# Optimization experiments

Hardware: AMD Instinct MI355X
Metric: run time of the kernel (lower is better)

## Reference

```python
import jax, jax.numpy as jnp
import numpy as np

EPS = 1e-12

def _l2norm(v, axis=-1):
    n = jnp.sqrt(jnp.sum(v * v, axis=axis, keepdims=True))
    return v / jnp.maximum(n, EPS)

def setup_inputs() -> dict:
    key = jax.random.key(0)
    ks = jax.random.split(key, 6)
    B, S, E, A = 256, 128, 768, 30
    x = jax.random.normal(ks[0], (B, S, E), dtype=jnp.float32)
    W_att = jax.random.normal(ks[1], (E, E), dtype=jnp.float32) * (1.0 / np.sqrt(E))
    b_att = jnp.zeros((E,), dtype=jnp.float32)
    W_red = jax.random.normal(ks[2], (E, A), dtype=jnp.float32) * (1.0 / np.sqrt(E))
    b_red = jnp.zeros((A,), dtype=jnp.float32)
    aspect_W = jax.random.normal(ks[3], (A, E), dtype=jnp.float32) * (1.0 / np.sqrt(E))
    # negatives: uniform over other batch elements (multinomial on ones - eye)
    idx = jax.random.randint(ks[4], (B, 10), 0, B - 1)
    neg_idx = (idx + (idx >= jnp.arange(B)[:, None])).astype(jnp.int32)  # skip self
    return {"x": x, "W_att": W_att, "b_att": b_att, "W_red": W_red,
            "b_red": b_red, "aspect_W": aspect_W, "neg_idx": neg_idx}

def reference(x, W_att, b_att, W_red, b_red, aspect_W, neg_idx):
    # --- LuongAttention(general): query = mean over seq ---
    q = x.mean(axis=1)                                   # [B,E]
    qW = q @ W_att + b_att                               # [B,E]
    scores = jnp.einsum('bse,be->bs', x, qW)             # [B,S]
    attn = jax.nn.softmax(scores, axis=-1)
    z_s = jnp.einsum('bs,bse->be', attn, x)              # attended sentence vec [B,E]
    # --- reduction + reconstruction ---
    composition = jax.nn.softmax(z_s @ W_red + b_red, axis=-1)  # [B,A]
    reconstructed = composition @ aspect_W                      # [B,E]
    # --- max-margin loss with gathered negatives ---
    r_s = _l2norm(reconstructed)                         # F.normalize
    z_n = z_s[neg_idx]                                   # [B,10,E] gather
    pos = jnp.einsum('be,be->b', z_s, r_s)[:, None]      # [B,1]
    negs = jnp.einsum('bne,be->bn', z_n, r_s)            # [B,10]
    J = 1.0 - pos + negs
    margin_loss = jnp.mean(jnp.maximum(J, 0.0))
    # --- orthogonal regularization on aspect embeddings ---
    T_n = _l2norm(aspect_W, axis=1)                      # [A,E]
    G = T_n @ T_n.T - jnp.eye(aspect_W.shape[0], dtype=aspect_W.dtype)
    reg = jnp.sqrt(jnp.sum(G * G))                       # Frobenius norm
    loss = reg + margin_loss
    return (z_s, reconstructed, loss)
```

## Files before the change

### kernel.cpp

```cpp
#include <hip/hip_runtime.h>
#include <hip/hip_bf16.h>
#include <hip/hip_fp16.h>
#include <math.h>

#define B 256
#define S 128
#define E 768
#define E4 192
#define NA 30
#define NNEG 10

#define K2_KC 96
#define K2_KR 192

__device__ __forceinline__ float dot4(float4 a, float4 b) {
    return a.x * b.x + a.y * b.y + a.z * b.z + a.w * b.w;
}
__device__ __forceinline__ float wave_reduce_sum(float v) {
#pragma unroll
    for (int off = 32; off; off >>= 1) v += __shfl_down(v, off);
    return v;
}
__device__ __forceinline__ float wave_reduce_max(float v) {
#pragma unroll
    for (int off = 32; off; off >>= 1) v = fmaxf(v, __shfl_down(v, off));
    return v;
}
__device__ __forceinline__ float4 h4_to_f4(uint2 p) {
    __half2* ph = (__half2*)&p;
    float2 f0 = __half22float2(ph[0]);
    float2 f1 = __half22float2(ph[1]);
    return make_float4(f0.x, f0.y, f1.x, f1.y);
}

template <int USE16>
__global__ __launch_bounds__(768) void mean_prep_kernel(const float* __restrict__ x,
                                                        const float* __restrict__ W_red,
                                                        const float* __restrict__ aspect_W,
                                                        float* __restrict__ q,
                                                        float* __restrict__ WredT,
                                                        float* __restrict__ invn,
                                                        __half* __restrict__ xh) {
    int bid = blockIdx.x;
    int tid = threadIdx.x;
    __shared__ __align__(16) float4 part[4][E4];
    __shared__ float red[12];

    if (bid < 2 * B) {
        int b = bid >> 1, half = bid & 1;
        int c = tid % E4;
        int g = tid / E4;
        const float4* xb = (const float4*)(x + (size_t)b * S * E);
        uint2* xhb = (uint2*)(xh + (size_t)b * S * E);
        int s0 = half * 64 + g * 16;
        float4 acc = make_float4(0.f, 0.f, 0.f, 0.f);
#pragma unroll 4
        for (int s = s0; s < s0 + 16; ++s) {
            float4 v = xb[(size_t)s * E4 + c];
            acc.x += v.x; acc.y += v.y; acc.z += v.z; acc.w += v.w;
            if (USE16) {
                __half2 h01 = __floats2half2_rn(v.x, v.y);
                __half2 h23 = __floats2half2_rn(v.z, v.w);
                uint2 pk;
                pk.x = *(unsigned int*)&h01;
                pk.y = *(unsigned int*)&h23;
                xhb[(size_t)s * E4 + c] = pk;
            }
        }
        part[g][c] = acc;
        __syncthreads();
        if (tid < E4) {
            float4 a0 = part[0][c], a1 = part[1][c], a2 = part[2][c], a3 = part[3][c];
            const float inv = 1.0f / (float)S;
            float4 r;
            r.x = (a0.x + a1.x + a2.x + a3.x) * inv;
            r.y = (a0.y + a1.y + a2.y + a3.y) * inv;
            r.z = (a0.z + a1.z + a2.z + a3.z) * inv;
            r.w = (a0.w + a1.w + a2.w + a3.w) * inv;
            ((float4*)q)[((size_t)half * B + b) * E4 + c] = r;
        }
    } else {
        int a = bid - 2 * B;
        WredT[(size_t)a * E + tid] = W_red[(size_t)tid * NA + a];
        int wave = tid >> 6, lane = tid & 63;
        float v = aspect_W[(size_t)a * E + tid];
        float ss = wave_reduce_sum(v * v);
        if (lane == 0) red[wave] = ss;
        __syncthreads();
        if (tid == 0) {
            float n = 0.f;
#pragma unroll
            for (int w = 0; w < 12; ++w) n += red[w];
            invn[a] = 1.0f / fmaxf(sqrtf(n), 1e-12f);
        }
    }
}

__global__ __launch_bounds__(256) void qw_partial_kernel(const float* __restrict__ q,
                                                         const float* __restrict__ W_att,
                                                         float* __restrict__ part) {
    int b0 = blockIdx.x * 64;
    int e0 = blockIdx.y * 64;
    int kz = blockIdx.z;
    int k0 = kz * K2_KR;
    int tid = threadIdx.x;

    __shared__ __align__(16) float qs[64][K2_KC + 4];
    __shared__ __align__(16) float ws[K2_KC][64];

    int r0 = (tid >> 3) * 2;
    int c0 = (tid & 7) * 8;

    float4 a00 = make_float4(0,0,0,0), a01 = make_float4(0,0,0,0);
    float4 a10 = make_float4(0,0,0,0), a11 = make_float4(0,0,0,0);

    for (int ch = 0; ch < 2; ++ch) {
        int kc0 = k0 + ch * K2_KC;
        {
            int row = tid >> 2, ks = (tid & 3) * 24;
            const float* src0 = q + (size_t)(b0 + row) * E + kc0 + ks;
            const float* src1 = src0 + (size_t)B * E;
#pragma unroll
            for (int j = 0; j < 6; ++j) {
                float4 v0 = *(const float4*)(src0 + 4 * j);
                float4 v1 = *(const float4*)(src1 + 4 * j);
                v0.x += v1.x; v0.y += v1.y; v0.z += v1.z; v0.w += v1.w;
                *(float4*)&qs[row][ks + 4 * j] = v0;
            }
        }
        for (int i = tid; i < K2_KC * 16; i += 256) {
            int row = i >> 4, e4 = (i & 15) * 4;
            *(float4*)&ws[row][e4] =
                *(const float4*)(W_att + (size_t)(kc0 + row) * E + e0 + e4);
        }
        __syncthreads();
#pragma unroll 4
        for (int k = 0; k < K2_KC; ++k) {
            float qa = qs[r0][k], qb = qs[r0 + 1][k];
            float4 w0 = *(const float4*)&ws[k][c0];
            float4 w1 = *(const float4*)&ws[k][c0 + 4];
            a00.x += qa * w0.x; a00.y += qa * w0.y; a00.z += qa * w0.z; a00.w += qa * w0.w;
            a01.x += qa * w1.x; a01.y += qa * w1.y; a01.z += qa * w1.z; a01.w += qa * w1.w;
            a10.x += qb * w0.x; a10.y += qb * w0.y; a10.z += qb * w0.z; a10.w += qb * w0.w;
            a11.x += qb * w1.x; a11.y += qb * w1.y; a11.z += qb * w1.z; a11.w += qb * w1.w;
        }
        __syncthreads();
    }
    float* dst = part + ((size_t)kz * B + b0 + r0) * E + e0 + c0;
    *(float4*)dst = a00; *(float4*)(dst + 4) = a01;
    *(float4*)(dst + E) = a10; *(float4*)(dst + E + 4) = a11;
}

template <int USE16>
__global__ __launch_bounds__(768) void attn_ortho_kernel(const float* __restrict__ x,
                                                         const __half* __restrict__ xh,
                                                         const float* __restrict__ part,
                                                         const float* __restrict__ b_att,
                                                         const float* __restrict__ aspect_W,
                                                         const float* __restrict__ invn,
                                                         float* __restrict__ z_s,
                                                         float* __restrict__ Gpart) {
    int bid = blockIdx.x;
    int tid = threadIdx.x, wave = tid >> 6, lane = tid & 63;
    __shared__ __align__(16) float4 qw4[E4];
    __shared__ float att[S];
    __shared__ float red[12];
    __shared__ __align__(16) float4 zpart[4][E4];

    if (bid >= B) {
        int i = bid - B;
        float inv_i = invn[i];
        if (tid < E4) {
            float4 v = ((const float4*)aspect_W)[(size_t)i * E4 + tid];
            v.x *= inv_i; v.y *= inv_i; v.z *= inv_i; v.w *= inv_i;
            qw4[tid] = v;
        }
        __syncthreads();
        float acc = 0.f;
        for (int j = wave; j < NA; j += 12) {
            const float4* aj = (const float4*)(aspect_W + (size_t)j * E);
            float d = 0.f;
#pragma unroll
            for (int jj = 0; jj < 3; ++jj)
                d += dot4(aj[lane + 64 * jj], qw4[lane + 64 * jj]);
            d = wave_reduce_sum(d);
            if (lane == 0) {
                float g = d * invn[j] - ((i == j) ? 1.f : 0.f);
                acc += g * g;
            }
        }
        if (lane == 0) red[wave] = acc;
        __syncthreads();
        if (tid == 0) {
            float s = 0.f;
#pragma unroll
            for (int w = 0; w < 12; ++w) s += red[w];
            Gpart[i] = s;
        }
        return;
    }

    int b = bid;
    const int N4 = B * E / 4;
    if (tid < E4) {
        const float4* p = (const float4*)part;
        size_t base = (size_t)b * E4 + tid;
        float4 s0 = p[base], s1 = p[base + N4], s2 = p[base + 2 * N4], s3 = p[base + 3 * N4];
        float4 bb = ((const float4*)b_att)[tid];
        float4 r;
        r.x = s0.x + s1.x + s2.x + s3.x + bb.x;
        r.y = s0.y + s1.y + s2.y + s3.y + bb.y;
        r.z = s0.z + s1.z + s2.z + s3.z + bb.z;
        r.w = s0.w + s1.w + s2.w + s3.w + bb.w;
        qw4[tid] = r;
    }
    __syncthreads();

    const float4* xb  = (const float4*)(x + (size_t)b * S * E);
    const uint2*  xhb = (const uint2*)(xh + (size_t)b * S * E);

    for (int p2 = wave; p2 < S / 2; p2 += 12) {
        int sA = 2 * p2;
        float dA = 0.f, dB = 0.f;
        if (USE16) {
            const uint2* rA = xhb + (size_t)sA * E4;
            const uint2* rB = rA + E4;
#pragma unroll
            for (int j = 0; j < 3; ++j) {
                float4 qv = qw4[lane + 64 * j];
                dA += dot4(h4_to_f4(rA[lane + 64 * j]), qv);
                dB += dot4(h4_to_f4(rB[lane + 64 * j]), qv);
            }
        } else {
            const float4* rA = xb + (size_t)sA * E4;
            const float4* rB = rA + E4;
#pragma unroll
            for (int j = 0; j < 3; ++j) {
                float4 qv = qw4[lane + 64 * j];
                dA += dot4(rA[lane + 64 * j], qv);
                dB += dot4(rB[lane + 64 * j], qv);
            }
        }
#pragma unroll
        for (int off = 32; off; off >>= 1) {
            dA += __shfl_down(dA, off);
            dB += __shfl_down(dB, off);
        }
        if (lane == 0) { att[sA] = dA; att[sA + 1] = dB; }
    }
    __syncthreads();

    float v = (tid < S) ? att[tid] : -3.4e38f;
    if (tid < S) {
        float m = wave_reduce_max(v);
        if (lane == 0) red[wave] = m;
    }
    __syncthreads();
    float gm = fmaxf(red[0], red[1]);
    float ex = 0.f;
    if (tid < S) {
        ex = expf(v - gm);
        float ss = wave_reduce_sum(ex);
        if (lane == 0) red[4 + wave] = ss;
    }
    __syncthreads();
    float tot = red[4] + red[5];
    if (tid < S) att[tid] = ex / tot;
    __syncthreads();

    int c = tid % E4, g = tid / E4;
    float4 acc = make_float4(0.f, 0.f, 0.f, 0.f);
    if (USE16) {
#pragma unroll 4
        for (int s = g * 32 + 31; s >= g * 32; --s) {
            float w = att[s];
            float4 xv = h4_to_f4(xhb[(size_t)s * E4 + c]);
            acc.x += w * xv.x; acc.y += w * xv.y; acc.z += w * xv.z; acc.w += w * xv.w;
        }
    } else {
#pragma unroll 4
        for (int s = g * 32 + 31; s >= g * 32; --s) {
            float w = att[s];
            float4 xv = xb[(size_t)s * E4 + c];
            acc.x += w * xv.x; acc.y += w * xv.y; acc.z += w * xv.z; acc.w += w * xv.w;
        }
    }
    zpart[g][c] = acc;
    __syncthreads();
    if (tid < E4) {
        float4 a0 = zpart[0][tid], a1 = zpart[1][tid], a2 = zpart[2][tid], a3 = zpart[3][tid];
        float4 r;
        r.x = a0.x + a1.x + a2.x + a3.x;
        r.y = a0.y + a1.y + a2.y + a3.y;
        r.z = a0.z + a1.z + a2.z + a3.z;
        r.w = a0.w + a1.w + a2.w + a3.w;
        ((float4*)z_s)[(size_t)b * E4 + tid] = r;
    }
}

__global__ __launch_bounds__(768) void recon_margin_kernel(const float* __restrict__ z_s,
                                                           const float* __restrict__ WredT,
                                                           const float* __restrict__ b_red,
                                                           const float* __restrict__ aspect_W,
                                                           const int* __restrict__ neg_idx,
                                                           float* __restrict__ recon,
                                                           float* __restrict__ mpart) {
    int b = blockIdx.x;
    int tid = threadIdx.x, wave = tid >> 6, lane = tid & 63;
    __shared__ __align__(16) float4 z4[E4];
    __shared__ float comp[NA];
    __shared__ __align__(16) float r_sh[E];
    __shared__ float red[12];
    __shared__ float dots[12];

    if (tid < E4) z4[tid] = ((const float4*)(z_s + (size_t)b * E))[tid];
    __syncthreads();

    for (int a = wave; a < NA; a += 12) {
        const float4* wr = (const float4*)(WredT + (size_t)a * E);
        float d = 0.f;
#pragma unroll
        for (int j = 0; j < 3; ++j)
            d += dot4(wr[lane + 64 * j], z4[lane + 64 * j]);
        d = wave_reduce_sum(d);
        if (lane == 0) comp[a] = d + b_red[a];
    }
    __syncthreads();

    if (wave == 0) {
        float v = (lane < NA) ? comp[lane] : -3.4e38f;
        float m = wave_reduce_max(v);
        m = __shfl(m, 0);
        float e = (lane < NA) ? expf(v - m) : 0.f;
        float ssum = wave_reduce_sum(e);
        ssum = __shfl(ssum, 0);
        if (lane < NA) comp[lane] = e / ssum;
    }
    __syncthreads();

    float r = 0.f;
    for (int a = 0; a < NA; ++a)
        r += comp[a] * aspect_W[(size_t)a * E + tid];
    recon[(size_t)b * E + tid] = r;
    r_sh[tid] = r;
    float sq = wave_reduce_sum(r * r);
    if (lane == 0) red[wave] = sq;
    __syncthreads();
    float tot = 0.f;
#pragma unroll
    for (int w = 0; w < 12; ++w) tot += red[w];
    float inv = 1.0f / fmaxf(sqrtf(tot), 1e-12f);

    if (wave <= NNEG) {
        int row = (wave == 0) ? b : neg_idx[b * NNEG + (wave - 1)];
        const float4* zr = (const float4*)(z_s + (size_t)row * E);
        const float4* rr = (const float4*)r_sh;
        float acc = 0.f;
#pragma unroll
        for (int j = 0; j < 3; ++j)
            acc += dot4(zr[lane + 64 * j], rr[lane + 64 * j]);
        acc = wave_reduce_sum(acc);
        if (lane == 0) dots[wave] = acc;
    }
    __syncthreads();
    if (tid == 0) {
        float pos = dots[0] * inv;
        float ssum = 0.f;
        for (int n = 1; n <= NNEG; ++n)
            ssum += fmaxf(1.f - pos + dots[n] * inv, 0.f);
        mpart[b] = ssum;
    }
}

__global__ __launch_bounds__(256) void loss_kernel(const float* __restrict__ Gpart,
                                                   const float* __restrict__ mpart,
                                                   float* __restrict__ loss_out) {
    int tid = threadIdx.x, wave = tid >> 6, lane = tid & 63;
    __shared__ float ra[4], rb[4];
    float fr = (tid < NA) ? Gpart[tid] : 0.f;
    fr = wave_reduce_sum(fr);
    if (lane == 0) ra[wave] = fr;
    float mp = mpart[tid];
    mp = wave_reduce_sum(mp);
    if (lane == 0) rb[wave] = mp;
    __syncthreads();
    if (tid == 0) {
        float frob = sqrtf(ra[0] + ra[1] + ra[2] + ra[3]);
        float msum = rb[0] + rb[1] + rb[2] + rb[3];
        loss_out[0] = frob + msum * (1.0f / (float)(B * NNEG));
    }
}

extern "C" void kernel_launch(void* const* d_in, const int* in_sizes, int n_in,
                              void* d_out, int out_size, void* d_ws, size_t ws_size,
                              hipStream_t stream) {
    const float* x        = (const float*)d_in[0];
    const float* W_att    = (const float*)d_in[1];
    const float* b_att    = (const float*)d_in[2];
    const float* W_red    = (const float*)d_in[3];
    const float* b_red    = (const float*)d_in[4];
    const float* aspect_W = (const float*)d_in[5];
    const int*   neg_idx  = (const int*)d_in[6];

    float* out   = (float*)d_out;
    float* z_s   = out;
    float* recon = out + (size_t)B * E;
    float* loss  = out + (size_t)2 * B * E;

    float* ws    = (float*)d_ws;
    float* q     = ws;
    float* part2 = q + (size_t)2 * B * E;
    float* WredT = part2 + (size_t)4 * B * E;
    float* invn  = WredT + (size_t)NA * E;
    float* Gpart = invn + 32;
    float* mpart = Gpart + 32;
    float* endf  = mpart + B;

    size_t base_floats = (size_t)(endf - ws);
    size_t need = base_floats * sizeof(float) + (size_t)B * S * E * sizeof(__half);
    bool use16 = (ws_size >= need);
    __half* xh = (__half*)(ws + base_floats);

    if (use16) {
        mean_prep_kernel<1><<<2 * B + NA, 768, 0, stream>>>(x, W_red, aspect_W, q, WredT, invn, xh);
        qw_partial_kernel<<<dim3(4, 12, 4), 256, 0, stream>>>(q, W_att, part2);
        attn_ortho_kernel<1><<<B + NA, 768, 0, stream>>>(x, xh, part2, b_att, aspect_W, invn, z_s, Gpart);
    } else {
        mean_prep_kernel<0><<<2 * B + NA, 768, 0, stream>>>(x, W_red, aspect_W, q, WredT, invn, xh);
        qw_partial_kernel<<<dim3(4, 12, 4), 256, 0, stream>>>(q, W_att, part2);
        attn_ortho_kernel<0><<<B + NA, 768, 0, stream>>>(x, xh, part2, b_att, aspect_W, invn, z_s, Gpart);
    }
    recon_margin_kernel<<<B, 768, 0, stream>>>(z_s, WredT, b_red, aspect_W, neg_idx, recon, mpart);
    loss_kernel<<<1, 256, 0, stream>>>(Gpart, mpart, loss);
}
```

Baseline: 68.68 us.

## Fuse attention scores, softmax and weighted sum with online softmax per wave

Rewrites the attention kernel so each of 8 waves streams 16 sequence rows once, computing scores and accumulating the softmax-weighted sum in registers with a running max and rescaling. The per-wave partials are merged at the end. This removes the second pass over x (read once instead of twice) and several block barriers, at the cost of more registers per thread and a change of block size from 768 to 512 threads.

Result: no change. 67.76 us (-1.3%).

```diff
diff --git a/kernel.cpp b/kernel.cpp
--- a/kernel.cpp
+++ b/kernel.cpp
@@ -152,7 +152,7 @@
 }
 
 template <int USE16>
-__global__ __launch_bounds__(768) void attn_ortho_kernel(const float* __restrict__ x,
+__global__ __launch_bounds__(512) void attn_ortho_kernel(const float* __restrict__ x,
                                                          const __half* __restrict__ xh,
                                                          const float* __restrict__ part,
                                                          const float* __restrict__ b_att,
@@ -163,9 +163,9 @@
     int bid = blockIdx.x;
     int tid = threadIdx.x, wave = tid >> 6, lane = tid & 63;
     __shared__ __align__(16) float4 qw4[E4];
-    __shared__ float att[S];
-    __shared__ float red[12];
-    __shared__ __align__(16) float4 zpart[4][E4];
+    __shared__ __align__(16) float4 zw[8][E4];
+    __shared__ float wm[8], wl[8];
+    __shared__ float red[8];
 
     if (bid >= B) {
         int i = bid - B;
@@ -177,7 +177,7 @@
         }
         __syncthreads();
         float acc = 0.f;
-        for (int j = wave; j < NA; j += 12) {
+        for (int j = wave; j < NA; j += 8) {
             const float4* aj = (const float4*)(aspect_W + (size_t)j * E);
             float d = 0.f;
 #pragma unroll
@@ -194,7 +194,7 @@
         if (tid == 0) {
             float s = 0.f;
 #pragma unroll
-            for (int w = 0; w < 12; ++w) s += red[w];
+            for (int w = 0; w < 8; ++w) s += red[w];
             Gpart[i] = s;
         }
         return;
@@ -216,85 +216,79 @@
     }
     __syncthreads();
 
+    float4 q0 = qw4[lane], q1 = qw4[lane + 64], q2 = qw4[lane + 128];
+
+    float m = -3.4e38f, l = 0.f;
+    float4 a0 = make_float4(0.f, 0.f, 0.f, 0.f);
+    float4 a1 = a0, a2 = a0;
+
+    const uint2*  xhb = (const uint2*)(xh + (size_t)b * S * E);
     const float4* xb  = (const float4*)(x + (size_t)b * S * E);
-    const uint2*  xhb = (const uint2*)(xh + (size_t)b * S * E);
-
-    for (int p2 = wave; p2 < S / 2; p2 += 12) {
-        int sA = 2 * p2;
-        float dA = 0.f, dB = 0.f;
+    int s0 = wave * 16;
+
+#pragma unroll
+    for (int i = 0; i < 16; i += 2) {
+        float4 xA0, xA1, xA2, xB0, xB1, xB2;
         if (USE16) {
-            const uint2* rA = xhb + (size_t)sA * E4;
+            const uint2* rA = xhb + (size_t)(s0 + i) * E4;
             const uint2* rB = rA + E4;
-#pragma unroll
-            for (int j = 0; j < 3; ++j) {
-                float4 qv = qw4[lane + 64 * j];
-                dA += dot4(h4_to_f4(rA[lane + 64 * j]), qv);
-                dB += dot4(h4_to_f4(rB[lane + 64 * j]), qv);
-            }
+            xA0 = h4_to_f4(rA[lane]); xA1 = h4_to_f4(rA[lane + 64]); xA2 = h4_to_f4(rA[lane + 128]);
+            xB0 = h4_to_f4(rB[lane]); xB1 = h4_to_f4(rB[lane + 64]); xB2 = h4_to_f4(rB[lane + 128]);
         } else {
-            const float4* rA = xb + (size_t)sA * E4;
+            const float4* rA = xb + (size_t)(s0 + i) * E4;
             const float4* rB = rA + E4;
-#pragma unroll
-            for (int j = 0; j < 3; ++j) {
-                float4 qv = qw4[lane + 64 * j];
-                dA += dot4(rA[lane + 64 * j], qv);
-                dB += dot4(rB[lane + 64 * j], qv);
-            }
-        }
+            xA0 = rA[lane]; xA1 = rA[lane + 64]; xA2 = rA[lane + 128];
+            xB0 = rB[lane]; xB1 = rB[lane + 64]; xB2 = rB[lane + 128];
+        }
+        float dA = dot4(xA0, q0) + dot4(xA1, q1) + dot4(xA2, q2);
+        float dB = dot4(xB0, q0) + dot4(xB1, q1) + dot4(xB2, q2);
 #pragma unroll
         for (int off = 32; off; off >>= 1) {
-            dA += __shfl_down(dA, off);
-            dB += __shfl_down(dB, off);
-        }
-        if (lane == 0) { att[sA] = dA; att[sA + 1] = dB; }
-    }
-    __syncthreads();
-
-    float v = (tid < S) ? att[tid] : -3.4e38f;
-    if (tid < S) {
-        float m = wave_reduce_max(v);
-        if (lane == 0) red[wave] = m;
-    }
-    __syncthreads();
-    float gm = fmaxf(red[0], red[1]);
-    float ex = 0.f;
-    if (tid < S) {
-        ex = expf(v - gm);
-        float ss = wave_reduce_sum(ex);
-        if (lane == 0) red[4 + wave] = ss;
-    }
-    __syncthreads();
-    float tot = red[4] + red[5];
-    if (tid < S) att[tid] = ex / tot;
-    __syncthreads();
-
-    int c = tid % E4, g = tid / E4;
-    float4 acc = make_float4(0.f, 0.f, 0.f, 0.f);
-    if (USE16) {
-#pragma unroll 4
-        for (int s = g * 32 + 31; s >= g * 32; --s) {
-            float w = att[s];
-            float4 xv = h4_to_f4(xhb[(size_t)s * E4 + c]);
-            acc.x += w * xv.x; acc.y += w * xv.y; acc.z += w * xv.z; acc.w += w * xv.w;
-        }
-    } else {
-#pragma unroll 4
-        for (int s = g * 32 + 31; s >= g * 32; --s) {
-            float w = att[s];
-            float4 xv = xb[(size_t)s * E4 + c];
-            acc.x += w * xv.x; acc.y += w * xv.y; acc.z += w * xv.z; acc.w += w * xv.w;
-        }
-    }
-    zpart[g][c] = acc;
-    __syncthreads();
+            dA += __shfl_xor(dA, off);
+            dB += __shfl_xor(dB, off);
+        }
+        float tm = fmaxf(m, fmaxf(dA, dB));
+        float sc = __expf(m - tm);
+        float eA = __expf(dA - tm);
+        float eB = __expf(dB - tm);
+        l = l * sc + eA + eB;
+        a0.x = a0.x * sc + eA * xA0.x + eB * xB0.x;
+        a0.y = a0.y * sc + eA * xA0.y + eB * xB0.y;
+        a0.z = a0.z * sc + eA * xA0.z + eB * xB0.z;
+        a0.w = a0.w * sc + eA * xA0.w + eB * xB0.w;
+        a1.x = a1.x * sc + eA * xA1.x + eB * xB1.x;
+        a1.y = a1.y * sc + eA * xA1.y + eB * xB1.y;
+        a1.z = a1.z * sc + eA * xA1.z + eB * xB1.z;
+        a1.w = a1.w * sc + eA * xA1.w + eB * xB1.w;
+        a2.x = a2.x * sc + eA * xA2.x + eB * xB2.x;
+        a2.y = a2.y * sc + eA * xA2.y + eB * xB2.y;
+        a2.z = a2.z * sc + eA * xA2.z + eB * xB2.z;
+        a2.w = a2.w * sc + eA * xA2.w + eB * xB2.w;
+        m = tm;
+    }
+
+    zw[wave][lane] = a0;
+    zw[wave][lane + 64] = a1;
+    zw[wave][lane + 128] = a2;
+    if (lane == 0) { wm[wave] = m; wl[wave] = l; }
+    __syncthreads();
+
     if (tid < E4) {
-        float4 a0 = zpart[0][tid], a1 = zpart[1][tid], a2 = zpart[2][tid], a3 = zpart[3][tid];
-        float4 r;
-        r.x = a0.x + a1.x + a2.x + a3.x;
-        r.y = a0.y + a1.y + a2.y + a3.y;
-        r.z = a0.z + a1.z + a2.z + a3.z;
-        r.w = a0.w + a1.w + a2.w + a3.w;
-        ((float4*)z_s)[(size_t)b * E4 + tid] = r;
+        float M = wm[0];
+#pragma unroll
+        for (int w = 1; w < 8; ++w) M = fmaxf(M, wm[w]);
+        float L = 0.f;
+        float4 z = make_float4(0.f, 0.f, 0.f, 0.f);
+#pragma unroll
+        for (int w = 0; w < 8; ++w) {
+            float f = __expf(wm[w] - M);
+            float4 a = zw[w][tid];
+            z.x += f * a.x; z.y += f * a.y; z.z += f * a.z; z.w += f * a.w;
+            L += f * wl[w];
+        }
+        float invL = 1.0f / L;
+        z.x *= invL; z.y *= invL; z.z *= invL; z.w *= invL;
+        ((float4*)z_s)[(size_t)b * E4 + tid] = z;
     }
 }
 
@@ -424,11 +418,11 @@
     if (use16) {
         mean_prep_kernel<1><<<2 * B + NA, 768, 0, stream>>>(x, W_red, aspect_W, q, WredT, invn, xh);
         qw_partial_kernel<<<dim3(4, 12, 4), 256, 0, stream>>>(q, W_att, part2);
-        attn_ortho_kernel<1><<<B + NA, 768, 0, stream>>>(x, xh, part2, b_att, aspect_W, invn, z_s, Gpart);
+        attn_ortho_kernel<1><<<B + NA, 512, 0, stream>>>(x, xh, part2, b_att, aspect_W, invn, z_s, Gpart);
     } else {
         mean_prep_kernel<0><<<2 * B + NA, 768, 0, stream>>>(x, W_red, aspect_W, q, WredT, invn, xh);
         qw_partial_kernel<<<dim3(4, 12, 4), 256, 0, stream>>>(q, W_att, part2);
-        attn_ortho_kernel<0><<<B + NA, 768, 0, stream>>>(x, xh, part2, b_att, aspect_W, invn, z_s, Gpart);
+        attn_ortho_kernel<0><<<B + NA, 512, 0, stream>>>(x, xh, part2, b_att, aspect_W, invn, z_s, Gpart);
     }
     recon_margin_kernel<<<B, 768, 0, stream>>>(z_s, WredT, b_red, aspect_W, neg_idx, recon, mpart);
     loss_kernel<<<1, 256, 0, stream>>>(Gpart, mpart, loss);
```
